# Kernel optimization log

Measured on AMD Instinct MI355X. Metric: run time of the kernel, lower is better.

The kernel has to match this reference:

```python
import jax, jax.numpy as jnp
import numpy as np

B, U, P = 32, 64, 8          # dialogues, utterances per dialogue, parties per dialogue
V, D, L = 32000, 300, 256    # vocab, emb_dim, sentence length
H, S = 5, 5                  # n_heads, n_steps
NP = 200                     # global number of parties
MAXLEN = 252
NT = B * (U + P)             # total nodes in batched graph


def setup_inputs() -> dict:
    key = jax.random.key(0)
    ks = iter(jax.random.split(key, 48))
    rn = lambda shape, s=0.02: jax.random.normal(next(ks), shape, jnp.float32) * s
    x = jax.random.randint(next(ks), (B * U, L), 0, V, dtype=jnp.int32)
    ps_local = np.array(jax.random.randint(next(ks), (B, U), 0, P, dtype=jnp.int32))
    # build batched dialogue graph (sequential utterance chain + utterance<->party edges)
    src, dst = [], []
    for g in range(B):
        off = g * (U + P)
        for i in range(U - 1):
            src += [off + i, off + i + 1]; dst += [off + i + 1, off + i]
        for i in range(U):
            q = off + U + int(ps_local[g, i])
            src += [off + i, q]; dst += [q, off + i]
    src = jnp.asarray(np.array(src, np.int32)); dst = jnp.asarray(np.array(dst, np.int32))
    node_ids = np.arange(NT).reshape(B, U + P)
    u_idx = jnp.asarray(node_ids[:, :U].reshape(-1).astype(np.int32))
    q_idx = jnp.asarray(node_ids[:, U:].reshape(-1).astype(np.int32))
    lid = jnp.tile(jnp.arange(U, dtype=jnp.int32), B)
    pids = jax.random.randint(next(ks), (B * P,), 0, NP, dtype=jnp.int32)
    py = jax.random.normal(next(ks), (B,), jnp.float32)
    return dict(
        x=x, src=src, dst=dst, u_idx=u_idx, q_idx=q_idx, lid=lid, pids=pids, py=py,
        word_W=rn((V, D), 1.0),
        conv_w3=rn((100, 1, 3, D)), conv_b3=rn((100,)),
        conv_w4=rn((100, 1, 4, D)), conv_b4=rn((100,)),
        conv_w5=rn((100, 1, 5, D)), conv_b5=rn((100,)),
        party_W=rn((NP, D), 1.0), pos_W=rn((MAXLEN, D)),
        gat_fc=rn((S, D, H * D)), gat_al=rn((S, H, D)), gat_ar=rn((S, H, D)),
        gat_res=rn((S, D, H * D)), gat_b=rn((S, H * D)),
        pa_W=rn((D, D)), pa_b=rn((D,)), pa_c=rn((D,)),
        sa_W=rn((D, D)), sa_b=rn((D,)), sa_c=rn((D,)),
        v_W=rn((1, D)), v_b=rn((D,)),
        out_W=rn((3 * D, 1)), out_b=rn((1,)))


def _text_cnn(emb, cw, cb):
    # emb [N,1,L,D], cw [100,1,w,D] -> valid conv [N,100,L-w+1,1] -> global max pool
    y = jax.lax.conv_general_dilated(emb, cw, (1, 1), 'VALID',
                                     dimension_numbers=('NCHW', 'OIHW', 'NCHW'))
    y = y + cb[None, :, None, None]
    return jnp.max(y, axis=(2, 3))  # [N,100]


def _ctx_attn(xb, W, b, c):
    # xb [B,K,D]; ContextAttention(batch=False) applied per dialogue: softmax over K
    h = jnp.tanh(xb @ W + b)
    a = jax.nn.softmax(h @ c, axis=1)          # [B,K]
    return jnp.einsum('bk,bkd->bd', a, xb)


def reference(x, src, dst, u_idx, q_idx, lid, pids, py,
              word_W, conv_w3, conv_b3, conv_w4, conv_b4, conv_w5, conv_b5,
              party_W, pos_W, gat_fc, gat_al, gat_ar, gat_res, gat_b,
              pa_W, pa_b, pa_c, sa_W, sa_b, sa_c, v_W, v_b, out_W, out_b):
    # text CNN utterance embedding
    emb = word_W[x][:, None, :, :]                       # [Nu,1,L,D]
    wx = jnp.concatenate([_text_cnn(emb, conv_w3, conv_b3),
                          _text_cnn(emb, conv_w4, conv_b4),
                          _text_cnn(emb, conv_w5, conv_b5)], axis=1)  # [Nu,300]
    # node features: utterances (+ positional), parties from party embedding
    feat = jnp.zeros((NT, D), wx.dtype)
    feat = feat.at[u_idx].set(wx + pos_W[lid])
    feat = feat.at[q_idx].set(party_W[pids])
    # n_steps GATConv layers (DGL semantics, residual + bias), mean over heads
    h = feat
    for i in range(S):
        z = (h @ gat_fc[i]).reshape(NT, H, D)            # [NT,H,D]
        el = jnp.einsum('nhd,hd->nh', z, gat_al[i])
        er = jnp.einsum('nhd,hd->nh', z, gat_ar[i])
        e = jax.nn.leaky_relu(el[src] + er[dst], 0.2)    # [E,H]
        m = jax.ops.segment_max(e, dst, num_segments=NT)
        ee = jnp.exp(e - m[dst])
        den = jax.ops.segment_sum(ee, dst, num_segments=NT)
        alpha = ee / den[dst]                            # edge softmax per dst
        agg = jax.ops.segment_sum(alpha[:, :, None] * z[src], dst, num_segments=NT)
        out = agg + (h @ gat_res[i]).reshape(NT, H, D) + gat_b[i].reshape(H, D)
        h = jnp.mean(out, axis=1)                        # [NT,D] (dropout is identity in eval)
    # per-dialogue context-attention pooling over party / sentence nodes
    hu = h[u_idx].reshape(B, U, D)
    hq = h[q_idx].reshape(B, P, D)
    px = _ctx_attn(hq, pa_W, pa_b, pa_c)
    sx = _ctx_attn(hu, sa_W, sa_b, sa_c)
    ox = jnp.concatenate([px, sx, py[:, None] @ v_W + v_b], axis=-1)  # [B,900]
    return ox @ out_W + out_b                            # [B,1]
```

## Files before the change

kernel.cpp:

```cpp
#include <hip/hip_runtime.h>
#include <stdint.h>

#define NUTT 2048
#define NNODE 2304
#define NE 8128

typedef __attribute__((ext_vector_type(8))) short short8;
typedef __attribute__((ext_vector_type(16))) float float16;

__device__ __forceinline__ float16 MFMA(short8 a, short8 b, float16 c) {
  return __builtin_amdgcn_mfma_f32_32x32x16_bf16(a, b, c, 0, 0, 0);
}

__device__ __forceinline__ unsigned short f2b(float f) {
  unsigned int u = __builtin_bit_cast(unsigned int, f);
  u = (u + 0x7FFFu + ((u >> 16) & 1u)) >> 16;
  return (unsigned short)u;
}
__device__ __forceinline__ float b2f(unsigned short h) {
  unsigned int u = ((unsigned int)h) << 16;
  return __builtin_bit_cast(float, u);
}

#define OFF_WW   0u
#define OFF_BCNN 19200000u
#define OFF_BGAT 20183040u
#define OFF_BSA  29521920u
#define OFF_BPA  29716480u
#define OFF_WX   29911040u
#define OFF_H16  32368640u
#define OFF_Z    33806336u
#define OFF_EL   47962112u
#define OFF_ER   48008192u
#define OFF_CNT  48054272u
#define OFF_CUR  48063488u
#define OFF_PTR  48072704u
#define OFF_EID  48082176u

__global__ void pack_wordW(const float* __restrict__ src, unsigned short* __restrict__ dst) {
  int i4 = (blockIdx.x * 256 + threadIdx.x) * 4;
  if (i4 >= 9600000) return;
  const float4 v = *(const float4*)(src + i4);
  uint2 o;
  o.x = (unsigned int)f2b(v.x) | ((unsigned int)f2b(v.y) << 16);
  o.y = (unsigned int)f2b(v.z) | ((unsigned int)f2b(v.w) << 16);
  *(uint2*)(dst + i4) = o;
}

__global__ void pack_cnnB(const float* __restrict__ w3, const float* __restrict__ w4,
                          const float* __restrict__ w5, unsigned short* __restrict__ out) {
  int i = blockIdx.x * 256 + threadIdx.x;
  if (i >= 491520) return;
  int width, local; const float* cw;
  if (i < 122880)      { width = 3; local = i;          cw = w3; }
  else if (i < 286720) { width = 4; local = i - 122880; cw = w4; }
  else                 { width = 5; local = i - 286720; cw = w5; }
  int KS = 20 * width;
  int per_nt = KS * 512;
  int nt = local / per_nt;
  int rem = local - nt * per_nt;
  int ks = rem >> 9;
  int lr = rem & 511;
  int lane = lr >> 3, j = lr & 7;
  int col = nt * 32 + (lane & 31);
  int k = ks * 16 + 8 * (lane >> 5) + j;
  int tap = k / 320, koff = k - tap * 320;
  float v = 0.f;
  if (col < 100 && koff < 300) v = cw[(col * width + tap) * 300 + koff];
  out[i] = f2b(v);
}

__global__ void pack_gatB(const float* __restrict__ fc, const float* __restrict__ res,
                          unsigned short* __restrict__ out) {
  int i = blockIdx.x * 256 + threadIdx.x;
  if (i >= 4669440) return;
  int layer = i / 933888;
  int rem = i - layer * 933888;
  int nt = rem / (19 * 512);
  int r2 = rem - nt * (19 * 512);
  int ks = r2 >> 9;
  int lr = r2 & 511;
  int lane = lr >> 3, j = lr & 7;
  int col = nt * 32 + (lane & 31);
  int k = ks * 16 + 8 * (lane >> 5) + j;
  float v = 0.f;
  if (k < 300) {
    if (col < 1500)      v = fc[((size_t)layer * 300 + k) * 1500 + col];
    else if (col < 3000) v = res[((size_t)layer * 300 + k) * 1500 + (col - 1500)];
  }
  out[i] = f2b(v);
}

__global__ void pack_poolB(const float* __restrict__ W, unsigned short* __restrict__ out) {
  int i = blockIdx.x * 256 + threadIdx.x;
  if (i >= 97280) return;
  int nt = i / (19 * 512);
  int r2 = i - nt * (19 * 512);
  int ks = r2 >> 9;
  int lr = r2 & 511;
  int lane = lr >> 3, j = lr & 7;
  int col = nt * 32 + (lane & 31);
  int k = ks * 16 + 8 * (lane >> 5) + j;
  float v = 0.f;
  if (k < 300 && col < 300) v = W[k * 300 + col];
  out[i] = f2b(v);
}

__global__ void csr_zero(int* cnt, int* cur) {
  int i = blockIdx.x * 256 + threadIdx.x;
  if (i < NNODE) { cnt[i] = 0; cur[i] = 0; }
}
__global__ void csr_count(const int* __restrict__ dst, int* cnt) {
  int e = blockIdx.x * 256 + threadIdx.x;
  if (e < NE) atomicAdd(&cnt[dst[e]], 1);
}
__global__ void csr_scan(const int* __restrict__ cnt, int* __restrict__ ptr) {
  __shared__ int part[256];
  __shared__ int loc[NNODE];
  int t = threadIdx.x;
  int s = 0;
  for (int k = 0; k < 9; ++k) { loc[t * 9 + k] = s; s += cnt[t * 9 + k]; }
  part[t] = s;
  __syncthreads();
  for (int off = 1; off < 256; off <<= 1) {
    int add = (t >= off) ? part[t - off] : 0;
    __syncthreads();
    part[t] += add;
    __syncthreads();
  }
  int base = part[t] - s;
  for (int k = 0; k < 9; ++k) ptr[t * 9 + k] = base + loc[t * 9 + k];
  if (t == 255) ptr[NNODE] = part[255];
}
__global__ void csr_scatter(const int* __restrict__ dst, const int* __restrict__ ptr,
                            int* cur, int* __restrict__ eid) {
  int e = blockIdx.x * 256 + threadIdx.x;
  if (e < NE) {
    int d = dst[e];
    int pos = atomicAdd(&cur[d], 1);
    eid[ptr[d] + pos] = e;
  }
}

template<int W, int WSEC>
__device__ __forceinline__ void cnn_section(const char* sm, float* scratch,
    const unsigned short* Bsec, const float* bias, float* wxrow, int tid) {
  int lane = tid & 63, wave = tid >> 6;
  int l31 = lane & 31, g = lane >> 5;
  int Mblk = wave >> 2, nt = wave & 3;
  const int KS = 20 * W;
  float16 acc[4] = {};
  const char* bptr = (const char*)Bsec + (size_t)(nt * KS) * 1024 + lane * 16;
  int rbase = Mblk * 128 + l31;
  for (int j = 0; j < W; ++j) {
    int q0 = rbase + j;       q0 = (q0 > 255 ? 255 : q0) * 624;
    int q1 = rbase + 32 + j;  q1 = (q1 > 255 ? 255 : q1) * 624;
    int q2 = rbase + 64 + j;  q2 = (q2 > 255 ? 255 : q2) * 624;
    int q3 = rbase + 96 + j;  q3 = (q3 > 255 ? 255 : q3) * 624;
    #pragma unroll 4
    for (int kl = 0; kl < 20; ++kl) {
      int kb = kl * 32 + 16 * g;
      short8 a0 = *(const short8*)(sm + q0 + kb);
      short8 a1 = *(const short8*)(sm + q1 + kb);
      short8 a2 = *(const short8*)(sm + q2 + kb);
      short8 a3 = *(const short8*)(sm + q3 + kb);
      short8 bb = *(const short8*)(bptr);
      bptr += 1024;
      acc[0] = MFMA(a0, bb, acc[0]);
      acc[1] = MFMA(a1, bb, acc[1]);
      acc[2] = MFMA(a2, bb, acc[2]);
      acc[3] = MFMA(a3, bb, acc[3]);
    }
  }
  float cm = -3.0e38f;
  #pragma unroll
  for (int mt = 0; mt < 4; ++mt) {
    #pragma unroll
    for (int r = 0; r < 16; ++r) {
      int row = Mblk * 128 + mt * 32 + (r & 3) + 8 * (r >> 2) + 4 * g;
      float v = acc[mt][r];
      if (row <= 256 - W && v > cm) cm = v;
    }
  }
  cm = fmaxf(cm, __shfl_xor(cm, 32));
  if (lane < 32) scratch[(Mblk * 4 + nt) * 32 + lane] = cm;
  __syncthreads();
  if (tid < 128) {
    int ntt = tid >> 5, c = tid & 31;
    int f = ntt * 32 + c;
    if (f < 100) {
      float v = fmaxf(scratch[ntt * 32 + c], scratch[(4 + ntt) * 32 + c]);
      wxrow[WSEC * 100 + f] = v + bias[f];
    }
  }
  __syncthreads();
}

__global__ __launch_bounds__(512, 2) void cnn_kernel(
    const int* __restrict__ x, const unsigned short* __restrict__ wW,
    const unsigned short* __restrict__ Bcnn,
    const float* __restrict__ cb3, const float* __restrict__ cb4, const float* __restrict__ cb5,
    float* __restrict__ wx) {
  extern __shared__ char sm[];
  int n = blockIdx.x, tid = threadIdx.x;
  float* scratch = (float*)(sm + 159808);
  if (tid < 16) *(int*)(sm + 159744 + tid * 4) = 0;
  const int* xr = x + n * 256;
  for (int i = tid; i < 19968; i += 512) {
    int r = i / 78, c = i - r * 78;
    uint2 v; v.x = 0u; v.y = 0u;
    if (c < 75) {
      int tok = xr[r];
      v = *(const uint2*)((const char*)wW + (size_t)tok * 600 + c * 8);
    }
    *(uint2*)(sm + r * 624 + c * 8) = v;
  }
  __syncthreads();
  float* wxrow = wx + (size_t)n * 300;
  cnn_section<3, 0>(sm, scratch, Bcnn,           cb3, wxrow, tid);
  cnn_section<4, 1>(sm, scratch, Bcnn + 122880,  cb4, wxrow, tid);
  cnn_section<5, 2>(sm, scratch, Bcnn + 286720,  cb5, wxrow, tid);
}

__global__ void feat_kernel(const float* __restrict__ wx, const float* __restrict__ posW,
                            const int* __restrict__ lid, const float* __restrict__ partyW,
                            const int* __restrict__ pids, const int* __restrict__ u_idx,
                            const int* __restrict__ q_idx, unsigned short* __restrict__ h16) {
  int b = blockIdx.x, t = threadIdx.x;
  int node = (b < NUTT) ? u_idx[b] : q_idx[b - NUTT];
  for (int d = t; d < 312; d += 64) {
    float v = 0.f;
    if (d < 300)
      v = (b < NUTT) ? (wx[(size_t)b * 300 + d] + posW[(size_t)lid[b] * 300 + d])
                     : partyW[(size_t)pids[b - NUTT] * 300 + d];
    h16[(size_t)node * 312 + d] = (d < 300) ? f2b(v) : (unsigned short)0;
  }
}

__global__ __launch_bounds__(512, 2) void gat_mm(
    const unsigned short* __restrict__ h16, const unsigned short* __restrict__ Bg,
    unsigned short* __restrict__ z) {
  extern __shared__ char sm[];
  int tid = threadIdx.x, lane = tid & 63, wave = tid >> 6;
  int WGm = blockIdx.x, WGn = blockIdx.y;
  const char* srcp = (const char*)h16 + (size_t)WGm * 79872;
  for (int i = tid; i < 4992; i += 512)
    *(uint4*)(sm + i * 16) = *(const uint4*)(srcp + (size_t)i * 16);
  __syncthreads();
  int l31 = lane & 31, g = lane >> 5;
  int Mblk = wave >> 2, Nblk = wave & 3;
  float16 acc[2][2] = {};
  const char* a0 = sm + (Mblk * 64 + l31) * 624 + 16 * g;
  const char* a1 = a0 + 32 * 624;
  const char* b0 = (const char*)Bg + (size_t)((WGn * 8 + Nblk * 2) * 19) * 1024 + lane * 16;
  const char* b1 = b0 + 19 * 1024;
  #pragma unroll 2
  for (int ks = 0; ks < 19; ++ks) {
    short8 A0 = *(const short8*)(a0 + ks * 32);
    short8 A1 = *(const short8*)(a1 + ks * 32);
    short8 B0 = *(const short8*)(b0 + (size_t)ks * 1024);
    short8 B1 = *(const short8*)(b1 + (size_t)ks * 1024);
    acc[0][0] = MFMA(A0, B0, acc[0][0]);
    acc[0][1] = MFMA(A0, B1, acc[0][1]);
    acc[1][0] = MFMA(A1, B0, acc[1][0]);
    acc[1][1] = MFMA(A1, B1, acc[1][1]);
  }
  #pragma unroll
  for (int mi = 0; mi < 2; ++mi)
    #pragma unroll
    for (int ni = 0; ni < 2; ++ni)
      #pragma unroll
      for (int r = 0; r < 16; ++r) {
        int row = WGm * 128 + Mblk * 64 + mi * 32 + (r & 3) + 8 * (r >> 2) + 4 * g;
        int col = WGn * 256 + (Nblk * 2 + ni) * 32 + l31;
        z[(size_t)row * 3072 + col] = f2b(acc[mi][ni][r]);
      }
}

__global__ void gat_edge1(const unsigned short* __restrict__ z,
                          const float* __restrict__ al, const float* __restrict__ ar,
                          float* __restrict__ el, float* __restrict__ er) {
  int node = blockIdx.x * 4 + (threadIdx.x >> 6);
  if (node >= NNODE) return;
  int lane = threadIdx.x & 63;
  for (int h = 0; h < 5; ++h) {
    float accl = 0.f, accr = 0.f;
    for (int d = lane; d < 300; d += 64) {
      float zv = b2f(z[(size_t)node * 3072 + h * 300 + d]);
      accl += zv * al[h * 300 + d];
      accr += zv * ar[h * 300 + d];
    }
    for (int s = 32; s; s >>= 1) {
      accl += __shfl_xor(accl, s);
      accr += __shfl_xor(accr, s);
    }
    if (lane == 0) { el[node * 5 + h] = accl; er[node * 5 + h] = accr; }
  }
}

__global__ __launch_bounds__(320) void gat_edge2(
    const unsigned short* __restrict__ z, const float* __restrict__ el,
    const float* __restrict__ er, const float* __restrict__ gb,
    const int* __restrict__ ptr, const int* __restrict__ eidl,
    const int* __restrict__ srcA, unsigned short* __restrict__ h16out) {
  int dstn = blockIdx.x;
  int tid = threadIdx.x, h = tid >> 6, lane = tid & 63;
  __shared__ float lds5[5][304];
  int p0 = ptr[dstn], deg = ptr[dstn + 1] - p0;
  float ee = 0.f, den = 0.f;
  int sj = 0;
  if (deg > 0) {
    float s = -3.0e38f;
    if (lane < deg) {
      int e = eidl[p0 + lane];
      sj = srcA[e];
      float sv = el[sj * 5 + h] + er[dstn * 5 + h];
      s = (sv >= 0.f) ? sv : 0.2f * sv;
    }
    float m = s;
    for (int t = 32; t; t >>= 1) m = fmaxf(m, __shfl_xor(m, t));
    ee = (lane < deg) ? __expf(s - m) : 0.f;
    den = ee;
    for (int t = 32; t; t >>= 1) den += __shfl_xor(den, t);
  }
  for (int it = 0; it < 5; ++it) {
    int d = lane + it * 64;
    float acc = 0.f;
    if (deg > 0) {
      for (int e = 0; e < deg; ++e) {
        float w = __shfl(ee, e);
        int srow = __shfl(sj, e);
        if (d < 300) acc += w * b2f(z[(size_t)srow * 3072 + h * 300 + d]);
      }
      acc /= den;
    }
    if (d < 300) {
      float res = b2f(z[(size_t)dstn * 3072 + 1500 + h * 300 + d]);
      lds5[h][d] = acc + res + gb[h * 300 + d];
    }
  }
  __syncthreads();
  if (tid < 312) {
    float v = 0.f;
    if (tid < 300)
      v = 0.2f * (lds5[0][tid] + lds5[1][tid] + lds5[2][tid] + lds5[3][tid] + lds5[4][tid]);
    h16out[(size_t)dstn * 312 + tid] = (tid < 300) ? f2b(v) : (unsigned short)0;
  }
}

__device__ __forceinline__ void ctx_attn(const char* XB, int mtiles, int Kvalid,
    const unsigned short* Bw, const float* bias, const float* cvec,
    float* T, float* AA, float* OUT, int tid) {
  int lane = tid & 63, wave = tid >> 6;
  int l31 = lane & 31, g = lane >> 5;
  int ntasks = mtiles * 10;
  for (int t = wave; t < ntasks; t += 8) {
    int nt, mt;
    if (mtiles == 2) { nt = t >> 1; mt = t & 1; } else { nt = t; mt = 0; }
    float16 acc = {};
    const char* ap = XB + (mt * 32 + l31) * 624 + 16 * g;
    const char* bp = (const char*)Bw + (size_t)(nt * 19) * 1024 + lane * 16;
    for (int ks = 0; ks < 19; ++ks) {
      short8 A = *(const short8*)(ap + ks * 32);
      short8 Bv = *(const short8*)(bp + (size_t)ks * 1024);
      acc = MFMA(A, Bv, acc);
    }
    int col = nt * 32 + l31;
    if (col < 300) {
      float bc = bias[col];
      #pragma unroll
      for (int r = 0; r < 16; ++r) {
        int row = mt * 32 + (r & 3) + 8 * (r >> 2) + 4 * g;
        T[row * 305 + col] = tanhf(acc[r] + bc);
      }
    }
  }
  __syncthreads();
  if (tid < 64) {
    float lg = -3.0e38f;
    if (tid < Kvalid) {
      lg = 0.f;
      for (int d = 0; d < 300; ++d) lg += T[tid * 305 + d] * cvec[d];
    }
    AA[tid] = lg;
  }
  __syncthreads();
  if (wave == 0) {
    float v = AA[lane];
    float m = v;
    for (int s2 = 32; s2; s2 >>= 1) m = fmaxf(m, __shfl_xor(m, s2));
    float e = (lane < Kvalid) ? __expf(v - m) : 0.f;
    float s = e;
    for (int s2 = 32; s2; s2 >>= 1) s += __shfl_xor(s, s2);
    AA[lane] = e / s;
  }
  __syncthreads();
  if (tid < 300) {
    float acc = 0.f;
    for (int k = 0; k < Kvalid; ++k)
      acc += AA[k] * b2f(*(const unsigned short*)(XB + k * 624 + tid * 2));
    OUT[tid] = acc;
  }
  __syncthreads();
}

__global__ __launch_bounds__(512) void pool_kernel(
    const unsigned short* __restrict__ h16,
    const int* __restrict__ u_idx, const int* __restrict__ q_idx,
    const float* __restrict__ py,
    const unsigned short* __restrict__ Bsa, const unsigned short* __restrict__ Bpa,
    const float* __restrict__ sab, const float* __restrict__ sac,
    const float* __restrict__ pab, const float* __restrict__ pac,
    const float* __restrict__ vW, const float* __restrict__ vb,
    const float* __restrict__ outW, const float* __restrict__ outb,
    float* __restrict__ dout) {
  extern __shared__ char sm[];
  int b = blockIdx.x, tid = threadIdx.x;
  char* HU = sm;
  char* HQ = sm + 39936;
  float* T   = (float*)(sm + 59904);
  float* AA  = (float*)(sm + 137984);
  float* PX  = (float*)(sm + 138240);
  float* SX  = (float*)(sm + 139456);
  float* RED = (float*)(sm + 140672);
  for (int i = tid; i < 64 * 78; i += 512) {
    int r = i / 78, c = i - r * 78;
    int node = u_idx[b * 64 + r];
    *(uint2*)(HU + r * 624 + c * 8) =
        *(const uint2*)((const char*)h16 + (size_t)node * 624 + c * 8);
  }
  for (int i = tid; i < 32 * 78; i += 512) {
    int r = i / 78, c = i - r * 78;
    uint2 v; v.x = 0u; v.y = 0u;
    if (r < 8) {
      int node = q_idx[b * 8 + r];
      v = *(const uint2*)((const char*)h16 + (size_t)node * 624 + c * 8);
    }
    *(uint2*)(HQ + r * 624 + c * 8) = v;
  }
  __syncthreads();
  ctx_attn(HU, 2, 64, Bsa, sab, sac, T, AA, SX, tid);
  ctx_attn(HQ, 1, 8,  Bpa, pab, pac, T, AA, PX, tid);
  float contrib = 0.f;
  if (tid < 300) {
    float pv = py[b] * vW[tid] + vb[tid];
    contrib = PX[tid] * outW[tid] + SX[tid] * outW[300 + tid] + pv * outW[600 + tid];
  }
  RED[tid] = contrib;
  __syncthreads();
  for (int s = 256; s > 0; s >>= 1) {
    if (tid < s) RED[tid] += RED[tid + s];
    __syncthreads();
  }
  if (tid == 0) dout[b] = RED[0] + outb[0];
}

extern "C" void kernel_launch(void* const* d_in, const int* in_sizes, int n_in,
                              void* d_out, int out_size, void* d_ws, size_t ws_size,
                              hipStream_t stream) {
  (void)in_sizes; (void)n_in; (void)out_size; (void)ws_size;
  const int*   x       = (const int*)d_in[0];
  const int*   srcA    = (const int*)d_in[1];
  const int*   dstA    = (const int*)d_in[2];
  const int*   u_idx   = (const int*)d_in[3];
  const int*   q_idx   = (const int*)d_in[4];
  const int*   lid     = (const int*)d_in[5];
  const int*   pids    = (const int*)d_in[6];
  const float* py      = (const float*)d_in[7];
  const float* word_W  = (const float*)d_in[8];
  const float* cw3     = (const float*)d_in[9];
  const float* cb3     = (const float*)d_in[10];
  const float* cw4     = (const float*)d_in[11];
  const float* cb4     = (const float*)d_in[12];
  const float* cw5     = (const float*)d_in[13];
  const float* cb5     = (const float*)d_in[14];
  const float* party_W = (const float*)d_in[15];
  const float* pos_W   = (const float*)d_in[16];
  const float* gat_fc  = (const float*)d_in[17];
  const float* gat_al  = (const float*)d_in[18];
  const float* gat_ar  = (const float*)d_in[19];
  const float* gat_res = (const float*)d_in[20];
  const float* gat_b   = (const float*)d_in[21];
  const float* pa_W    = (const float*)d_in[22];
  const float* pa_b    = (const float*)d_in[23];
  const float* pa_c    = (const float*)d_in[24];
  const float* sa_W    = (const float*)d_in[25];
  const float* sa_b    = (const float*)d_in[26];
  const float* sa_c    = (const float*)d_in[27];
  const float* v_W     = (const float*)d_in[28];
  const float* v_b     = (const float*)d_in[29];
  const float* out_W   = (const float*)d_in[30];
  const float* out_b   = (const float*)d_in[31];

  char* ws = (char*)d_ws;
  unsigned short* wW16 = (unsigned short*)(ws + OFF_WW);
  unsigned short* Bcnn = (unsigned short*)(ws + OFF_BCNN);
  unsigned short* Bgat = (unsigned short*)(ws + OFF_BGAT);
  unsigned short* Bsa  = (unsigned short*)(ws + OFF_BSA);
  unsigned short* Bpa  = (unsigned short*)(ws + OFF_BPA);
  float*          wx   = (float*)(ws + OFF_WX);
  unsigned short* h16  = (unsigned short*)(ws + OFF_H16);
  unsigned short* z    = (unsigned short*)(ws + OFF_Z);
  float*          el   = (float*)(ws + OFF_EL);
  float*          er   = (float*)(ws + OFF_ER);
  int*            cnt  = (int*)(ws + OFF_CNT);
  int*            cur  = (int*)(ws + OFF_CUR);
  int*            ptr  = (int*)(ws + OFF_PTR);
  int*            eid  = (int*)(ws + OFF_EID);

  (void)hipFuncSetAttribute((const void*)cnn_kernel,
      hipFuncAttributeMaxDynamicSharedMemorySize, 160832);
  (void)hipFuncSetAttribute((const void*)gat_mm,
      hipFuncAttributeMaxDynamicSharedMemorySize, 79872);
  (void)hipFuncSetAttribute((const void*)pool_kernel,
      hipFuncAttributeMaxDynamicSharedMemorySize, 142720);

  pack_wordW<<<dim3(9375), dim3(256), 0, stream>>>(word_W, wW16);
  pack_cnnB<<<dim3(1920), dim3(256), 0, stream>>>(cw3, cw4, cw5, Bcnn);
  pack_gatB<<<dim3(18240), dim3(256), 0, stream>>>(gat_fc, gat_res, Bgat);
  pack_poolB<<<dim3(380), dim3(256), 0, stream>>>(sa_W, Bsa);
  pack_poolB<<<dim3(380), dim3(256), 0, stream>>>(pa_W, Bpa);

  csr_zero<<<dim3(9), dim3(256), 0, stream>>>(cnt, cur);
  csr_count<<<dim3(32), dim3(256), 0, stream>>>(dstA, cnt);
  csr_scan<<<dim3(1), dim3(256), 0, stream>>>(cnt, ptr);
  csr_scatter<<<dim3(32), dim3(256), 0, stream>>>(dstA, ptr, cur, eid);

  cnn_kernel<<<dim3(2048), dim3(512), 160832, stream>>>(x, wW16, Bcnn, cb3, cb4, cb5, wx);
  feat_kernel<<<dim3(NNODE), dim3(64), 0, stream>>>(wx, pos_W, lid, party_W, pids,
                                                    u_idx, q_idx, h16);
  for (int l = 0; l < 5; ++l) {
    gat_mm<<<dim3(18, 12), dim3(512), 79872, stream>>>(h16, Bgat + (size_t)l * 933888, z);
    gat_edge1<<<dim3(576), dim3(256), 0, stream>>>(z, gat_al + l * 1500, gat_ar + l * 1500,
                                                   el, er);
    gat_edge2<<<dim3(NNODE), dim3(320), 0, stream>>>(z, el, er, gat_b + l * 1500,
                                                     ptr, eid, srcA, h16);
  }
  pool_kernel<<<dim3(32), dim3(512), 142720, stream>>>(
      h16, u_idx, q_idx, py, Bsa, Bpa, sa_b, sa_c, pa_b, pa_c,
      v_W, v_b, out_W, out_b, (float*)d_out);
}
```

Baseline: 1.087 ms.

## Retile CNN MFMA to 2x2 wave tiles and trim K padding to 304

Each wave in the text-CNN kernel now computes a 64-row by 64-column output tile (2x2 MFMA blocks) instead of 128 rows by 32 columns. This halves the A-fragment LDS reads per MFMA while doubling the B reads from global memory. The per-tap K padding drops from 320 to 304 (19 k-steps instead of 20), cutting wasted MFMAs and shrinking the LDS row stride from 624 to 608 bytes. The inner loops are fully unrolled, and the max-reduction is rewritten to combine four row-block partials per filter. The 608-byte stride may raise LDS bank conflicts, and the full unroll adds register pressure under launch bounds of 512 threads with 2 blocks per CU.

After: 1.302 ms. 19.7% more time.

```diff
diff --git a/kernel.cpp b/kernel.cpp
--- a/kernel.cpp
+++ b/kernel.cpp
@@ -50,12 +50,12 @@
 __global__ void pack_cnnB(const float* __restrict__ w3, const float* __restrict__ w4,
                           const float* __restrict__ w5, unsigned short* __restrict__ out) {
   int i = blockIdx.x * 256 + threadIdx.x;
-  if (i >= 491520) return;
+  if (i >= 466944) return;
   int width, local; const float* cw;
-  if (i < 122880)      { width = 3; local = i;          cw = w3; }
-  else if (i < 286720) { width = 4; local = i - 122880; cw = w4; }
-  else                 { width = 5; local = i - 286720; cw = w5; }
-  int KS = 20 * width;
+  if (i < 116736)      { width = 3; local = i;          cw = w3; }
+  else if (i < 272384) { width = 4; local = i - 116736; cw = w4; }
+  else                 { width = 5; local = i - 272384; cw = w5; }
+  int KS = 19 * width;
   int per_nt = KS * 512;
   int nt = local / per_nt;
   int rem = local - nt * per_nt;
@@ -64,7 +64,7 @@
   int lane = lr >> 3, j = lr & 7;
   int col = nt * 32 + (lane & 31);
   int k = ks * 16 + 8 * (lane >> 5) + j;
-  int tap = k / 320, koff = k - tap * 320;
+  int tap = k / 304, koff = k - tap * 304;
   float v = 0.f;
   if (col < 100 && koff < 300) v = cw[(col * width + tap) * 300 + koff];
   out[i] = f2b(v);
@@ -145,51 +145,60 @@
 template<int W, int WSEC>
 __device__ __forceinline__ void cnn_section(const char* sm, float* scratch,
     const unsigned short* Bsec, const float* bias, float* wxrow, int tid) {
+  const int KS = 19 * W;
   int lane = tid & 63, wave = tid >> 6;
   int l31 = lane & 31, g = lane >> 5;
-  int Mblk = wave >> 2, nt = wave & 3;
-  const int KS = 20 * W;
-  float16 acc[4] = {};
-  const char* bptr = (const char*)Bsec + (size_t)(nt * KS) * 1024 + lane * 16;
-  int rbase = Mblk * 128 + l31;
+  int Mblk = wave >> 1, ntp = wave & 1;
+  float16 acc[2][2] = {};
+  const char* bbase = (const char*)Bsec + (size_t)(ntp * 2 * KS) * 1024 + lane * 16;
+  int rbase = Mblk * 64 + l31;
+  int ks = 0;
+  #pragma unroll
   for (int j = 0; j < W; ++j) {
-    int q0 = rbase + j;       q0 = (q0 > 255 ? 255 : q0) * 624;
-    int q1 = rbase + 32 + j;  q1 = (q1 > 255 ? 255 : q1) * 624;
-    int q2 = rbase + 64 + j;  q2 = (q2 > 255 ? 255 : q2) * 624;
-    int q3 = rbase + 96 + j;  q3 = (q3 > 255 ? 255 : q3) * 624;
-    #pragma unroll 4
-    for (int kl = 0; kl < 20; ++kl) {
+    int q0 = rbase + j;       q0 = (q0 > 255 ? 255 : q0) * 608;
+    int q1 = rbase + 32 + j;  q1 = (q1 > 255 ? 255 : q1) * 608;
+    #pragma unroll
+    for (int kl = 0; kl < 19; ++kl) {
       int kb = kl * 32 + 16 * g;
       short8 a0 = *(const short8*)(sm + q0 + kb);
       short8 a1 = *(const short8*)(sm + q1 + kb);
-      short8 a2 = *(const short8*)(sm + q2 + kb);
-      short8 a3 = *(const short8*)(sm + q3 + kb);
-      short8 bb = *(const short8*)(bptr);
-      bptr += 1024;
-      acc[0] = MFMA(a0, bb, acc[0]);
-      acc[1] = MFMA(a1, bb, acc[1]);
-      acc[2] = MFMA(a2, bb, acc[2]);
-      acc[3] = MFMA(a3, bb, acc[3]);
-    }
-  }
-  float cm = -3.0e38f;
+      short8 b0 = *(const short8*)(bbase + (size_t)ks * 1024);
+      short8 b1 = *(const short8*)(bbase + (size_t)(KS + ks) * 1024);
+      ++ks;
+      acc[0][0] = MFMA(a0, b0, acc[0][0]);
+      acc[0][1] = MFMA(a0, b1, acc[0][1]);
+      acc[1][0] = MFMA(a1, b0, acc[1][0]);
+      acc[1][1] = MFMA(a1, b1, acc[1][1]);
+    }
+  }
+  float cm0 = -3.0e38f, cm1 = -3.0e38f;
   #pragma unroll
-  for (int mt = 0; mt < 4; ++mt) {
+  for (int mi = 0; mi < 2; ++mi) {
     #pragma unroll
     for (int r = 0; r < 16; ++r) {
-      int row = Mblk * 128 + mt * 32 + (r & 3) + 8 * (r >> 2) + 4 * g;
-      float v = acc[mt][r];
-      if (row <= 256 - W && v > cm) cm = v;
-    }
-  }
-  cm = fmaxf(cm, __shfl_xor(cm, 32));
-  if (lane < 32) scratch[(Mblk * 4 + nt) * 32 + lane] = cm;
+      int row = Mblk * 64 + mi * 32 + (r & 3) + 8 * (r >> 2) + 4 * g;
+      if (row <= 256 - W) {
+        float v0 = acc[mi][0][r], v1 = acc[mi][1][r];
+        if (v0 > cm0) cm0 = v0;
+        if (v1 > cm1) cm1 = v1;
+      }
+    }
+  }
+  cm0 = fmaxf(cm0, __shfl_xor(cm0, 32));
+  cm1 = fmaxf(cm1, __shfl_xor(cm1, 32));
+  if (lane < 32) {
+    scratch[wave * 64 + l31]      = cm0;
+    scratch[wave * 64 + 32 + l31] = cm1;
+  }
   __syncthreads();
   if (tid < 128) {
-    int ntt = tid >> 5, c = tid & 31;
-    int f = ntt * 32 + c;
+    int f = tid;
     if (f < 100) {
-      float v = fmaxf(scratch[ntt * 32 + c], scratch[(4 + ntt) * 32 + c]);
+      int ntp_f = f >> 6, rest = f & 63;
+      float v =        scratch[(0 * 2 + ntp_f) * 64 + rest];
+      v = fmaxf(v,     scratch[(1 * 2 + ntp_f) * 64 + rest]);
+      v = fmaxf(v,     scratch[(2 * 2 + ntp_f) * 64 + rest]);
+      v = fmaxf(v,     scratch[(3 * 2 + ntp_f) * 64 + rest]);
       wxrow[WSEC * 100 + f] = v + bias[f];
     }
   }
@@ -203,23 +212,22 @@
     float* __restrict__ wx) {
   extern __shared__ char sm[];
   int n = blockIdx.x, tid = threadIdx.x;
-  float* scratch = (float*)(sm + 159808);
-  if (tid < 16) *(int*)(sm + 159744 + tid * 4) = 0;
+  float* scratch = (float*)(sm + 155648);
   const int* xr = x + n * 256;
-  for (int i = tid; i < 19968; i += 512) {
-    int r = i / 78, c = i - r * 78;
+  for (int i = tid; i < 19456; i += 512) {
+    int r = i / 76, c = i - r * 76;
     uint2 v; v.x = 0u; v.y = 0u;
     if (c < 75) {
       int tok = xr[r];
       v = *(const uint2*)((const char*)wW + (size_t)tok * 600 + c * 8);
     }
-    *(uint2*)(sm + r * 624 + c * 8) = v;
+    *(uint2*)(sm + r * 608 + c * 8) = v;
   }
   __syncthreads();
   float* wxrow = wx + (size_t)n * 300;
   cnn_section<3, 0>(sm, scratch, Bcnn,           cb3, wxrow, tid);
-  cnn_section<4, 1>(sm, scratch, Bcnn + 122880,  cb4, wxrow, tid);
-  cnn_section<5, 2>(sm, scratch, Bcnn + 286720,  cb5, wxrow, tid);
+  cnn_section<4, 1>(sm, scratch, Bcnn + 116736,  cb4, wxrow, tid);
+  cnn_section<5, 2>(sm, scratch, Bcnn + 272384,  cb5, wxrow, tid);
 }
 
 __global__ void feat_kernel(const float* __restrict__ wx, const float* __restrict__ posW,
@@ -509,14 +517,14 @@
   int*            eid  = (int*)(ws + OFF_EID);
 
   (void)hipFuncSetAttribute((const void*)cnn_kernel,
-      hipFuncAttributeMaxDynamicSharedMemorySize, 160832);
+      hipFuncAttributeMaxDynamicSharedMemorySize, 157696);
   (void)hipFuncSetAttribute((const void*)gat_mm,
       hipFuncAttributeMaxDynamicSharedMemorySize, 79872);
   (void)hipFuncSetAttribute((const void*)pool_kernel,
       hipFuncAttributeMaxDynamicSharedMemorySize, 142720);
 
   pack_wordW<<<dim3(9375), dim3(256), 0, stream>>>(word_W, wW16);
-  pack_cnnB<<<dim3(1920), dim3(256), 0, stream>>>(cw3, cw4, cw5, Bcnn);
+  pack_cnnB<<<dim3(1824), dim3(256), 0, stream>>>(cw3, cw4, cw5, Bcnn);
   pack_gatB<<<dim3(18240), dim3(256), 0, stream>>>(gat_fc, gat_res, Bgat);
   pack_poolB<<<dim3(380), dim3(256), 0, stream>>>(sa_W, Bsa);
   pack_poolB<<<dim3(380), dim3(256), 0, stream>>>(pa_W, Bpa);
@@ -526,7 +534,7 @@
   csr_scan<<<dim3(1), dim3(256), 0, stream>>>(cnt, ptr);
   csr_scatter<<<dim3(32), dim3(256), 0, stream>>>(dstA, ptr, cur, eid);
 
-  cnn_kernel<<<dim3(2048), dim3(512), 160832, stream>>>(x, wW16, Bcnn, cb3, cb4, cb5, wx);
+  cnn_kernel<<<dim3(2048), dim3(512), 157696, stream>>>(x, wW16, Bcnn, cb3, cb4, cb5, wx);
   feat_kernel<<<dim3(NNODE), dim3(64), 0, stream>>>(wx, pos_W, lid, party_W, pids,
                                                     u_idx, q_idx, h16);
   for (int l = 0; l < 5; ++l) {
```
